# Kernel optimization log

Measured on AMD Instinct MI355X. Metric: run time of the kernel, lower is better.

Reference implementation:

```python
import jax, jax.numpy as jnp
import numpy as np

QMAX8 = 127.0  # 2**(8-1)-1


def quant1(x, scale):
    # 1-bit symmetric quant: s * sign(x), s = |scale| (per-group mean scale)
    return jnp.abs(scale) * jnp.sign(x)


def quant8(x, scale):
    s = jnp.maximum(jnp.abs(scale), 1e-8)
    q = jnp.clip(jnp.round(x / s), -QMAX8, QMAX8)
    return q * s


def setup_inputs() -> dict:
    key = jax.random.key(0)
    ks = jax.random.split(key, 5)
    p, j, k, m, l, n = 2, 32, 32, 32, 8, 32
    x = jax.random.normal(ks[0], (2, 1024, k * n), dtype=jnp.float32)
    Y_fp = jax.random.normal(ks[1], (p, j, k, m, l), dtype=jnp.float32)
    Z_fp = jax.random.normal(ks[2], (p, j, k, l, n), dtype=jnp.float32)
    A = jax.random.normal(ks[3], (p, j, k, 4), dtype=jnp.float32)
    bias = jax.random.normal(ks[4], (j * m,), dtype=jnp.float32)
    act_scale = jnp.full((1,), 0.001, dtype=jnp.float32)
    return {"x": x, "Y_fp": Y_fp, "Z_fp": Z_fp, "A": A, "bias": bias,
            "act_scale": act_scale}


def reference(x, Y_fp, Z_fp, A, bias, act_scale):
    p, j, k, m, l = Y_fp.shape
    n = Z_fp.shape[-1]
    orig_shape = x.shape[:-1]
    X = x.astype(jnp.float32)
    X = quant8(X, act_scale)  # activation quantization (act_bits=8)

    # per-(p,j,k) mean-abs scales over last two dims
    Y_scale = jnp.mean(jnp.abs(Y_fp), axis=(-2, -1), keepdims=True)
    Z_scale = jnp.mean(jnp.abs(Z_fp), axis=(-2, -1), keepdims=True)
    Y_q = quant1(Y_fp, Y_scale)  # (p,j,k,m,l)
    Z_q = quant1(Z_fp, Z_scale)  # (p,j,k,l,n)

    X_kn = X.reshape(-1, k, n)  # (B,k,n)
    T = jnp.einsum('bkn,pjkln->bpjkl', X_kn, Z_q)
    core = jnp.einsum('pjkml,bpjkl->bpjkm', Y_q, T)

    # quant_bias=True correction terms
    a = A[..., 0][None, ..., None]            # (1,p,j,k,1)
    out1 = jnp.sum(core * a, axis=(1, 3))     # (B,j,m)
    Y_sum = jnp.sum(Y_q, axis=-1)             # (p,j,k,m)
    B_coef = jnp.sum(A[..., 1][..., None] * Y_sum, axis=0)  # (j,k,m)
    Sx = jnp.sum(X_kn, axis=-1)               # (B,k)
    out2 = jnp.einsum('bk,jkm->bjm', Sx, B_coef)
    Zs = jnp.sum(Z_q, axis=-2)                # (p,j,k,n)
    Tz = jnp.einsum('bkn,pjkn->bpjk', X_kn, Zs)
    out3 = jnp.sum(Tz * A[..., 2][None], axis=(1, 3))[..., None]  # (B,j,1)
    D_coef = jnp.sum(A[..., 3], axis=0)       # (j,k)
    out4 = jnp.einsum('bk,jk->bj', Sx, D_coef)[..., None]          # (B,j,1)

    out_bjm = out1 + out2 + out3 + out4       # (B,j,m) via broadcast
    out_2d = out_bjm.reshape(-1, j * m) + bias
    out = out_2d.reshape(*orig_shape, j * m)
    return out.astype(x.dtype)
```

## Files before the change

kernel.cpp:

```cpp
#include <hip/hip_runtime.h>
#include <math.h>
#include <stdint.h>


typedef __attribute__((ext_vector_type(8))) short bf16x8;
typedef __attribute__((ext_vector_type(4))) float f32x4;
typedef __attribute__((ext_vector_type(4))) unsigned short us4;

__device__ __forceinline__ float fsign(float v) {
    return (v > 0.f) ? 1.f : ((v < 0.f) ? -1.f : 0.f);
}

__device__ __forceinline__ unsigned short f2bf(float f) {
    union { float f; uint32_t u; } c; c.f = f;
    uint32_t r = 0x7fffu + ((c.u >> 16) & 1u);
    return (unsigned short)((c.u + r) >> 16);
}

__device__ __forceinline__ void gl2lds16(const void* g, void* l) {
    __builtin_amdgcn_global_load_lds(
        (const __attribute__((address_space(1))) void*)g,
        (__attribute__((address_space(3))) void*)l, 16, 0, 0);
}

__global__ __launch_bounds__(256) void precompute_wt(
    const float* __restrict__ Y,
    const float* __restrict__ Z,
    const float* __restrict__ A,
    unsigned short* __restrict__ wt)
{
    __shared__ float sgy[256];
    __shared__ float sgz[256];
    __shared__ float wred[8];

    const int jk = blockIdx.x;
    const int jj = jk >> 5;
    const int kk = jk & 31;
    const int t  = threadIdx.x;
    const int n  = t & 31;
    const int mb = t >> 5;

    float acc[4] = {0.f, 0.f, 0.f, 0.f};

    for (int p = 0; p < 2; ++p) {
        const int base = ((p * 32 + jj) * 32 + kk);
        const float yv = Y[(size_t)base * 256 + t];
        const float zv = Z[(size_t)base * 256 + t];
        sgy[t] = fsign(yv);
        sgz[t] = fsign(zv);

        float ay = fabsf(yv), az = fabsf(zv);
        #pragma unroll
        for (int d = 1; d < 64; d <<= 1) {
            ay += __shfl_xor(ay, d, 64);
            az += __shfl_xor(az, d, 64);
        }
        if ((t & 63) == 0) {
            wred[(t >> 6) * 2 + 0] = ay;
            wred[(t >> 6) * 2 + 1] = az;
        }
        __syncthreads();

        const float sY = (wred[0] + wred[2] + wred[4] + wred[6]) * (1.f / 256.f);
        const float sZ = (wred[1] + wred[3] + wred[5] + wred[7]) * (1.f / 256.f);
        const float a0 = A[(size_t)base * 4 + 0];
        const float a1 = A[(size_t)base * 4 + 1];
        const float a2 = A[(size_t)base * 4 + 2];
        const float a3 = A[(size_t)base * 4 + 3];

        float zcol = 0.f;
        #pragma unroll
        for (int l = 0; l < 8; ++l) zcol += sgz[l * 32 + n];

        #pragma unroll
        for (int q = 0; q < 4; ++q) {
            const int m = mb + 8 * q;
            float ysum = 0.f, w = 0.f;
            #pragma unroll
            for (int l = 0; l < 8; ++l) {
                const float ys = sgy[m * 8 + l];
                ysum += ys;
                w += ys * sgz[l * 32 + n];
            }
            acc[q] += a0 * sY * sZ * w + a1 * sY * ysum + a2 * sZ * zcol + a3;
        }
        __syncthreads();
    }

    #pragma unroll
    for (int q = 0; q < 4; ++q) {
        const int m = mb + 8 * q;
        wt[(size_t)(jj * 32 + m) * 1024 + kk * 32 + n] = f2bf(acc[q]);
    }
}

__global__ __launch_bounds__(256) void quantize_x(
    const float* __restrict__ x, const float* __restrict__ act_scale,
    unsigned short* __restrict__ qx)
{
    const float s = fmaxf(fabsf(act_scale[0]), 1e-8f);
    const size_t i4 = (size_t)blockIdx.x * 256 + threadIdx.x;
    const float4 v = *(const float4*)(x + i4 * 4);
    us4 o;
    o.x = f2bf(fminf(fmaxf(rintf(v.x / s), -127.f), 127.f));
    o.y = f2bf(fminf(fmaxf(rintf(v.y / s), -127.f), 127.f));
    o.z = f2bf(fminf(fmaxf(rintf(v.z / s), -127.f), 127.f));
    o.w = f2bf(fminf(fmaxf(rintf(v.w / s), -127.f), 127.f));
    *(us4*)(qx + i4 * 4) = o;
}

__global__ __launch_bounds__(256) void gemm_mfma(
    const unsigned short* __restrict__ qx,
    const unsigned short* __restrict__ wt,
    const float* __restrict__ bias,
    const float* __restrict__ act_scale,
    float* __restrict__ out)
{
    __shared__ __align__(16) short lds[64 * 32 + 128 * 32];
    short* As = lds;
    short* Bs = lds + 64 * 32;

    const int tid  = threadIdx.x;
    const int lane = tid & 63;
    const int wave = tid >> 6;
    const int wm = wave >> 1;
    const int wn = wave & 1;
    const int rowBase = blockIdx.y * 64;
    const int colBase = blockIdx.x * 128;

    const float s = fmaxf(fabsf(act_scale[0]), 1e-8f);

    f32x4 acc[2][4];
    #pragma unroll
    for (int i = 0; i < 2; ++i)
        #pragma unroll
        for (int jx = 0; jx < 4; ++jx)
            acc[i][jx] = (f32x4)0.f;

    const unsigned short* agp =
        qx + (size_t)(rowBase + (tid >> 2)) * 1024 + (tid & 3) * 8;
    const unsigned short* bgp0 =
        wt + (size_t)(colBase + (tid >> 2)) * 1024 + (tid & 3) * 8;
    const unsigned short* bgp1 = bgp0 + (size_t)64 * 1024;

    char* const ldsc = (char*)lds;
    void* aw  = ldsc + wave * 1024;
    void* bw0 = ldsc + 4096 + wave * 1024;
    void* bw1 = ldsc + 4096 + 4096 + wave * 1024;

    const int q4  = lane >> 4;
    const int l16 = lane & 15;

    for (int k0 = 0; k0 < 1024; k0 += 32) {
        gl2lds16(agp  + k0, aw);
        gl2lds16(bgp0 + k0, bw0);
        gl2lds16(bgp1 + k0, bw1);
        __syncthreads();

        bf16x8 af[2], bfr[4];
        #pragma unroll
        for (int im = 0; im < 2; ++im)
            af[im] = *(const bf16x8*)&As[(wm * 32 + im * 16 + l16) * 32 + q4 * 8];
        #pragma unroll
        for (int in = 0; in < 4; ++in)
            bfr[in] = *(const bf16x8*)&Bs[(wn * 64 + in * 16 + l16) * 32 + q4 * 8];

        #pragma unroll
        for (int im = 0; im < 2; ++im)
            #pragma unroll
            for (int in = 0; in < 4; ++in)
                acc[im][in] = __builtin_amdgcn_mfma_f32_16x16x32_bf16(
                    af[im], bfr[in], acc[im][in], 0, 0, 0);

        __syncthreads();
    }

    #pragma unroll
    for (int im = 0; im < 2; ++im) {
        #pragma unroll
        for (int in = 0; in < 4; ++in) {
            const int col = colBase + wn * 64 + in * 16 + l16;
            const float b = bias[col];
            #pragma unroll
            for (int r = 0; r < 4; ++r) {
                const int row = rowBase + wm * 32 + im * 16 + q4 * 4 + r;
                out[(size_t)row * 1024 + col] = s * acc[im][in][r] + b;
            }
        }
    }
}

extern "C" void kernel_launch(void* const* d_in, const int* in_sizes, int n_in,
                              void* d_out, int out_size, void* d_ws, size_t ws_size,
                              hipStream_t stream) {
    const float* x         = (const float*)d_in[0];
    const float* Y_fp      = (const float*)d_in[1];
    const float* Z_fp      = (const float*)d_in[2];
    const float* A         = (const float*)d_in[3];
    const float* bias      = (const float*)d_in[4];
    const float* act_scale = (const float*)d_in[5];
    float* out = (float*)d_out;

    unsigned short* wt = (unsigned short*)d_ws;
    unsigned short* qx = (unsigned short*)((char*)d_ws + 2 * 1024 * 1024);

    precompute_wt<<<dim3(1024), dim3(256), 0, stream>>>(Y_fp, Z_fp, A, wt);
    quantize_x<<<dim3(2048), dim3(256), 0, stream>>>(x, act_scale, qx);
    gemm_mfma<<<dim3(8, 32), dim3(256), 0, stream>>>(qx, wt, bias, act_scale, out);
}
```

Baseline: 93.03 us.

## Fuse preprocessing kernels and double-buffer LDS tiles in MFMA GEMM

```diff
diff --git a/kernel.cpp b/kernel.cpp
--- a/kernel.cpp
+++ b/kernel.cpp
@@ -23,12 +23,34 @@
         (__attribute__((address_space(3))) void*)l, 16, 0, 0);
 }
 
-__global__ __launch_bounds__(256) void precompute_wt(
+__global__ __launch_bounds__(256) void fused_pre(
     const float* __restrict__ Y,
     const float* __restrict__ Z,
     const float* __restrict__ A,
-    unsigned short* __restrict__ wt)
+    const float* __restrict__ x,
+    const float* __restrict__ act_scale,
+    unsigned short* __restrict__ wt,
+    unsigned short* __restrict__ qx)
 {
+    const int t = threadIdx.x;
+
+    if (blockIdx.x >= 1024) {
+        const float s = fmaxf(fabsf(act_scale[0]), 1e-8f);
+        const int b2 = blockIdx.x - 1024;
+        #pragma unroll
+        for (int it = 0; it < 4; ++it) {
+            const size_t i4 = (size_t)b2 * 256 + t + (size_t)it * 131072;
+            const float4 v = *(const float4*)(x + i4 * 4);
+            us4 o;
+            o.x = f2bf(fminf(fmaxf(rintf(v.x / s), -127.f), 127.f));
+            o.y = f2bf(fminf(fmaxf(rintf(v.y / s), -127.f), 127.f));
+            o.z = f2bf(fminf(fmaxf(rintf(v.z / s), -127.f), 127.f));
+            o.w = f2bf(fminf(fmaxf(rintf(v.w / s), -127.f), 127.f));
+            *(us4*)(qx + i4 * 4) = o;
+        }
+        return;
+    }
+
     __shared__ float sgy[256];
     __shared__ float sgz[256];
     __shared__ float wred[8];
@@ -36,7 +58,6 @@
     const int jk = blockIdx.x;
     const int jj = jk >> 5;
     const int kk = jk & 31;
-    const int t  = threadIdx.x;
     const int n  = t & 31;
     const int mb = t >> 5;
 
@@ -94,21 +115,6 @@
     }
 }
 
-__global__ __launch_bounds__(256) void quantize_x(
-    const float* __restrict__ x, const float* __restrict__ act_scale,
-    unsigned short* __restrict__ qx)
-{
-    const float s = fmaxf(fabsf(act_scale[0]), 1e-8f);
-    const size_t i4 = (size_t)blockIdx.x * 256 + threadIdx.x;
-    const float4 v = *(const float4*)(x + i4 * 4);
-    us4 o;
-    o.x = f2bf(fminf(fmaxf(rintf(v.x / s), -127.f), 127.f));
-    o.y = f2bf(fminf(fmaxf(rintf(v.y / s), -127.f), 127.f));
-    o.z = f2bf(fminf(fmaxf(rintf(v.z / s), -127.f), 127.f));
-    o.w = f2bf(fminf(fmaxf(rintf(v.w / s), -127.f), 127.f));
-    *(us4*)(qx + i4 * 4) = o;
-}
-
 __global__ __launch_bounds__(256) void gemm_mfma(
     const unsigned short* __restrict__ qx,
     const unsigned short* __restrict__ wt,
@@ -116,9 +122,7 @@
     const float* __restrict__ act_scale,
     float* __restrict__ out)
 {
-    __shared__ __align__(16) short lds[64 * 32 + 128 * 32];
-    short* As = lds;
-    short* Bs = lds + 64 * 32;
+    __shared__ __align__(16) short lds[2 * 6144];
 
     const int tid  = threadIdx.x;
     const int lane = tid & 63;
@@ -144,18 +148,30 @@
     const unsigned short* bgp1 = bgp0 + (size_t)64 * 1024;
 
     char* const ldsc = (char*)lds;
-    void* aw  = ldsc + wave * 1024;
-    void* bw0 = ldsc + 4096 + wave * 1024;
-    void* bw1 = ldsc + 4096 + 4096 + wave * 1024;
-
     const int q4  = lane >> 4;
     const int l16 = lane & 15;
 
-    for (int k0 = 0; k0 < 1024; k0 += 32) {
-        gl2lds16(agp  + k0, aw);
-        gl2lds16(bgp0 + k0, bw0);
-        gl2lds16(bgp1 + k0, bw1);
+    {
+        char* b = ldsc;
+        gl2lds16(agp,  b + wave * 1024);
+        gl2lds16(bgp0, b + 4096 + wave * 1024);
+        gl2lds16(bgp1, b + 8192 + wave * 1024);
+    }
+
+    for (int kt = 0; kt < 32; ++kt) {
         __syncthreads();
+        const int cur = kt & 1;
+
+        if (kt + 1 < 32) {
+            const int k1 = (kt + 1) * 32;
+            char* b = ldsc + (cur ^ 1) * 12288;
+            gl2lds16(agp  + k1, b + wave * 1024);
+            gl2lds16(bgp0 + k1, b + 4096 + wave * 1024);
+            gl2lds16(bgp1 + k1, b + 8192 + wave * 1024);
+        }
+
+        const short* As = lds + cur * 6144;
+        const short* Bs = As + 2048;
 
         bf16x8 af[2], bfr[4];
         #pragma unroll
@@ -171,8 +187,6 @@
             for (int in = 0; in < 4; ++in)
                 acc[im][in] = __builtin_amdgcn_mfma_f32_16x16x32_bf16(
                     af[im], bfr[in], acc[im][in], 0, 0, 0);
-
-        __syncthreads();
     }
 
     #pragma unroll
@@ -204,7 +218,6 @@
     unsigned short* wt = (unsigned short*)d_ws;
     unsigned short* qx = (unsigned short*)((char*)d_ws + 2 * 1024 * 1024);
 
-    precompute_wt<<<dim3(1024), dim3(256), 0, stream>>>(Y_fp, Z_fp, A, wt);
-    quantize_x<<<dim3(2048), dim3(256), 0, stream>>>(x, act_scale, qx);
+    fused_pre<<<dim3(1536), dim3(256), 0, stream>>>(Y_fp, Z_fp, A, x, act_scale, wt, qx);
     gemm_mfma<<<dim3(8, 32), dim3(256), 0, stream>>>(qx, wt, bias, act_scale, out);
 }
```

Result: faster. 87.49 us (-6.0%).
